# Performance work log

Measured on AMD Instinct MI355X. Metric: run time of the kernel, lower is better.

The kernel has to match this reference:

```python
import jax, jax.numpy as jnp
import numpy as np

B, T, D = 32, 2048, 1024
MAX_NSEG = 128  # max_nsegments
# max_nframes == T (required by the mask @ x matmul in the original module)


def setup_inputs() -> dict:
    key = jax.random.key(0)
    k1, k2 = jax.random.split(key)
    x = jax.random.normal(k1, (B, T, D), dtype=jnp.float32)
    # sparse segment boundaries, ~60 segments per utterance (< MAX_NSEG)
    in_boundary = (jax.random.uniform(k2, (B, T + 1)) < 0.03).astype(jnp.int32)
    # original code prepends 0 if first boundary != 0; also close the last segment
    in_boundary = in_boundary.at[:, 0].set(1).at[:, -1].set(1)
    return {"x": x, "in_boundary": in_boundary}


def _build_mask(in_boundary, n_seg, n_frames):
    # boundary at index i starts a new segment at frame i; index T only ends the
    # last segment, so frames 0..T-1 use boundary[:, :T]. Force a boundary at 0
    # (the original prepends 0 to segment_times when missing).
    b = in_boundary[:, :n_frames].at[:, 0].set(1)
    seg_id = jnp.cumsum(b, axis=1) - 1                       # [B, T] segment index per frame
    onehot = jax.nn.one_hot(seg_id, n_seg, dtype=jnp.float32)  # [B, T, S]; seg_id >= S -> all-zero row
    counts = onehot.sum(axis=1)                              # [B, S] frames per segment
    inv = jnp.where(counts > 0, 1.0 / jnp.maximum(counts, 1.0), 0.0)
    mask = jnp.swapaxes(onehot, 1, 2) * inv[:, :, None]      # [B, S, T], rows sum to 1 (or 0)
    return mask


def reference(x, in_boundary):
    mask = _build_mask(in_boundary, MAX_NSEG, x.shape[1])
    pooled = jnp.einsum('bst,btd->bsd', mask, x)             # segment mean-pooling
    return pooled, mask.sum(-1), in_boundary
```

## Files before the change

kernel.cpp:

```cpp
#include <hip/hip_runtime.h>

#define NB 32
#define NT 2048
#define ND 1024
#define NS 128
#define CH 64
#define NQ (NT / CH)

typedef float f32x4 __attribute__((ext_vector_type(4)));

__device__ __forceinline__ void nt_store4(float* p, float a, float b, float c, float d) {
    f32x4 v = {a, b, c, d};
    __builtin_nontemporal_store(v, (f32x4*)p);
}

__global__ __launch_bounds__(256)
void seg_scan_kernel(const int* __restrict__ in_boundary,
                     int* __restrict__ sid,
                     int* __restrict__ seg_start,
                     int* __restrict__ seg_count,
                     float* __restrict__ out1,
                     float* __restrict__ out2)
{
    const int b    = blockIdx.x;
    const int tid  = threadIdx.x;
    const int lane = tid & 63;
    const int wid  = tid >> 6;
    const int* bd  = in_boundary + (size_t)b * (NT + 1);

    __shared__ int starts[NS + 1];
    __shared__ int wtot[4];

    for (int s = tid; s <= NS; s += 256) starts[s] = NT;

    const int t0 = tid * 8;
    int v[8];
    int local = 0;
#pragma unroll
    for (int j = 0; j < 8; ++j) {
        int t = t0 + j;
        int bit = (t == 0) ? 1 : bd[t];
        v[j] = bit;
        local += bit;
    }

    int incl = local;
#pragma unroll
    for (int off = 1; off < 64; off <<= 1) {
        int n = __shfl_up(incl, off, 64);
        if (lane >= off) incl += n;
    }
    if (lane == 63) wtot[wid] = incl;
    __syncthreads();

    int wpref = 0;
#pragma unroll
    for (int w = 0; w < 4; ++w)
        if (w < wid) wpref += wtot[w];
    const int excl = wpref + incl - local;

    int run = excl;
#pragma unroll
    for (int j = 0; j < 8; ++j) {
        run += v[j];
        int seg = run - 1;
        sid[(size_t)b * NT + t0 + j] = seg;
        if (v[j] && seg <= NS) starts[seg] = t0 + j;
    }
    __syncthreads();

    if (tid < NS) {
        int st = starts[tid];
        int c  = starts[tid + 1] - st;
        seg_start[b * NS + tid] = st;
        seg_count[b * NS + tid] = c;
        out1[b * NS + tid] = (c > 0) ? 1.0f : 0.0f;
    }

    for (int t = tid; t <= NT; t += 256)
        out2[(size_t)b * (NT + 1) + t] = (float)bd[t];
}

__global__ __launch_bounds__(256)
void pool_chunk_kernel(const float* __restrict__ x,
                       const int* __restrict__ sid,
                       const int* __restrict__ seg_start,
                       const int* __restrict__ seg_count,
                       float* __restrict__ partial,
                       float* __restrict__ pooled)
{
    const int q   = blockIdx.x;
    const int b   = blockIdx.y;
    const int tid = threadIdx.x;
    const int t0  = q * CH;

    __shared__ int sid_l[CH];
    if (tid < CH) sid_l[tid] = sid[(size_t)b * NT + t0 + tid];
    __syncthreads();
    const int s_first = sid_l[0];

    const float4* xp = (const float4*)(x + (size_t)b * NT * ND) + tid;

    float4 acc = make_float4(0.f, 0.f, 0.f, 0.f);
    int cur = s_first;

    auto flush = [&](int seg, const float4& a) {
        if (seg >= NS) return;
        const int st = seg_start[b * NS + seg];
        const int c  = seg_count[b * NS + seg];
        if (st >= t0 && st + c <= t0 + CH) {
            const float inv = 1.0f / (float)c;
            nt_store4(pooled + ((size_t)b * NS + seg) * ND + tid * 4,
                      a.x * inv, a.y * inv, a.z * inv, a.w * inv);
        } else {
            const int slot = (seg == s_first) ? 0 : 1;
            ((float4*)partial)[(((size_t)b * NQ + q) * 2 + slot) * (ND / 4) + tid] = a;
        }
    };

    for (int g = 0; g < CH / 8; ++g) {
        float4 v[8];
#pragma unroll
        for (int j = 0; j < 8; ++j)
            v[j] = xp[(size_t)(t0 + g * 8 + j) * (ND / 4)];
#pragma unroll
        for (int j = 0; j < 8; ++j) {
            int sg = sid_l[g * 8 + j];
            if (sg != cur) {
                flush(cur, acc);
                acc = make_float4(0.f, 0.f, 0.f, 0.f);
                cur = sg;
            }
            acc.x += v[j].x; acc.y += v[j].y; acc.z += v[j].z; acc.w += v[j].w;
        }
    }
    flush(cur, acc);
}

__global__ __launch_bounds__(256)
void combine_kernel(const int* __restrict__ seg_start,
                    const int* __restrict__ seg_count,
                    const float* __restrict__ partial,
                    float* __restrict__ pooled)
{
    const int s   = blockIdx.x;
    const int b   = blockIdx.y;
    const int tid = threadIdx.x;

    const int st = seg_start[b * NS + s];
    const int c  = seg_count[b * NS + s];
    float* out = pooled + ((size_t)b * NS + s) * ND + tid * 4;

    if (c <= 0) {
        nt_store4(out, 0.f, 0.f, 0.f, 0.f);
        return;
    }
    const int q0 = st / CH;
    const int q1 = (st + c - 1) / CH;
    if (q0 == q1) return;

    const float4* pp = (const float4*)partial + tid;
    const int slot0 = (st == q0 * CH) ? 0 : 1;
    float4 a = pp[(((size_t)b * NQ + q0) * 2 + slot0) * (ND / 4)];
    for (int q = q0 + 1; q <= q1; ++q) {
        float4 v = pp[(((size_t)b * NQ + q) * 2 + 0) * (ND / 4)];
        a.x += v.x; a.y += v.y; a.z += v.z; a.w += v.w;
    }
    const float inv = 1.0f / (float)c;
    nt_store4(out, a.x * inv, a.y * inv, a.z * inv, a.w * inv);
}

extern "C" void kernel_launch(void* const* d_in, const int* in_sizes, int n_in,
                              void* d_out, int out_size, void* d_ws, size_t ws_size,
                              hipStream_t stream) {
    const float* x           = (const float*)d_in[0];
    const int*   in_boundary = (const int*)d_in[1];

    float* pooled = (float*)d_out;
    float* out1   = pooled + (size_t)NB * NS * ND;
    float* out2   = out1 + (size_t)NB * NS;

    int*   sid       = (int*)d_ws;
    int*   seg_start = sid + (size_t)NB * NT;
    int*   seg_count = seg_start + NB * NS;
    float* partial   = (float*)(seg_count + NB * NS);

    seg_scan_kernel<<<NB, 256, 0, stream>>>(in_boundary, sid, seg_start,
                                            seg_count, out1, out2);
    pool_chunk_kernel<<<dim3(NQ, NB), 256, 0, stream>>>(x, sid, seg_start,
                                                        seg_count, partial, pooled);
    combine_kernel<<<dim3(NS, NB), 256, 0, stream>>>(seg_start, seg_count,
                                                     partial, pooled);
}
```

Before: 56.30 us.

## Fuse segment scan into pooling kernel, recomputing scan per chunk block

```diff
diff --git a/kernel.cpp b/kernel.cpp
--- a/kernel.cpp
+++ b/kernel.cpp
@@ -15,32 +15,48 @@
 }
 
 __global__ __launch_bounds__(256)
-void seg_scan_kernel(const int* __restrict__ in_boundary,
-                     int* __restrict__ sid,
-                     int* __restrict__ seg_start,
-                     int* __restrict__ seg_count,
-                     float* __restrict__ out1,
-                     float* __restrict__ out2)
+void fused_pool_kernel(const float* __restrict__ x,
+                       const int* __restrict__ in_boundary,
+                       int* __restrict__ seg_start_ws,
+                       int* __restrict__ seg_count_ws,
+                       float* __restrict__ partial,
+                       float* __restrict__ pooled,
+                       float* __restrict__ out1,
+                       float* __restrict__ out2)
 {
-    const int b    = blockIdx.x;
+    const int q    = blockIdx.x;
+    const int b    = blockIdx.y;
     const int tid  = threadIdx.x;
     const int lane = tid & 63;
     const int wid  = tid >> 6;
+    const int t0   = q * CH;
     const int* bd  = in_boundary + (size_t)b * (NT + 1);
+
+    const float4* xp = (const float4*)(x + (size_t)b * NT * ND) + tid;
+
+    float4 p0 = xp[(size_t)(t0 + 0) * (ND / 4)];
+    float4 p1 = xp[(size_t)(t0 + 1) * (ND / 4)];
+    float4 p2 = xp[(size_t)(t0 + 2) * (ND / 4)];
+    float4 p3 = xp[(size_t)(t0 + 3) * (ND / 4)];
+    float4 p4 = xp[(size_t)(t0 + 4) * (ND / 4)];
+    float4 p5 = xp[(size_t)(t0 + 5) * (ND / 4)];
+    float4 p6 = xp[(size_t)(t0 + 6) * (ND / 4)];
+    float4 p7 = xp[(size_t)(t0 + 7) * (ND / 4)];
 
     __shared__ int starts[NS + 1];
     __shared__ int wtot[4];
+    __shared__ int sid_all[NT];
 
     for (int s = tid; s <= NS; s += 256) starts[s] = NT;
 
-    const int t0 = tid * 8;
-    int v[8];
+    const int f0 = tid * 8;
+    int bv[8];
     int local = 0;
 #pragma unroll
     for (int j = 0; j < 8; ++j) {
-        int t = t0 + j;
+        int t = f0 + j;
         int bit = (t == 0) ? 1 : bd[t];
-        v[j] = bit;
+        bv[j] = bit;
         local += bit;
     }
 
@@ -62,52 +78,33 @@
     int run = excl;
 #pragma unroll
     for (int j = 0; j < 8; ++j) {
-        run += v[j];
+        run += bv[j];
         int seg = run - 1;
-        sid[(size_t)b * NT + t0 + j] = seg;
-        if (v[j] && seg <= NS) starts[seg] = t0 + j;
+        sid_all[f0 + j] = seg;
+        if (bv[j] && seg <= NS) starts[seg] = f0 + j;
     }
     __syncthreads();
 
-    if (tid < NS) {
-        int st = starts[tid];
-        int c  = starts[tid + 1] - st;
-        seg_start[b * NS + tid] = st;
-        seg_count[b * NS + tid] = c;
-        out1[b * NS + tid] = (c > 0) ? 1.0f : 0.0f;
+    if (q == 0) {
+        if (tid < NS) {
+            int st = starts[tid];
+            int c  = starts[tid + 1] - st;
+            seg_start_ws[b * NS + tid] = st;
+            seg_count_ws[b * NS + tid] = c;
+            out1[b * NS + tid] = (c > 0) ? 1.0f : 0.0f;
+        }
+        for (int t = tid; t <= NT; t += 256)
+            out2[(size_t)b * (NT + 1) + t] = (float)bd[t];
     }
 
-    for (int t = tid; t <= NT; t += 256)
-        out2[(size_t)b * (NT + 1) + t] = (float)bd[t];
-}
-
-__global__ __launch_bounds__(256)
-void pool_chunk_kernel(const float* __restrict__ x,
-                       const int* __restrict__ sid,
-                       const int* __restrict__ seg_start,
-                       const int* __restrict__ seg_count,
-                       float* __restrict__ partial,
-                       float* __restrict__ pooled)
-{
-    const int q   = blockIdx.x;
-    const int b   = blockIdx.y;
-    const int tid = threadIdx.x;
-    const int t0  = q * CH;
-
-    __shared__ int sid_l[CH];
-    if (tid < CH) sid_l[tid] = sid[(size_t)b * NT + t0 + tid];
-    __syncthreads();
-    const int s_first = sid_l[0];
-
-    const float4* xp = (const float4*)(x + (size_t)b * NT * ND) + tid;
-
+    const int s_first = sid_all[t0];
     float4 acc = make_float4(0.f, 0.f, 0.f, 0.f);
     int cur = s_first;
 
     auto flush = [&](int seg, const float4& a) {
         if (seg >= NS) return;
-        const int st = seg_start[b * NS + seg];
-        const int c  = seg_count[b * NS + seg];
+        const int st = starts[seg];
+        const int c  = starts[seg + 1] - st;
         if (st >= t0 && st + c <= t0 + CH) {
             const float inv = 1.0f / (float)c;
             nt_store4(pooled + ((size_t)b * NS + seg) * ND + tid * 4,
@@ -118,21 +115,29 @@
         }
     };
 
-    for (int g = 0; g < CH / 8; ++g) {
+    auto consume = [&](int t, const float4& v) {
+        int sg = sid_all[t];
+        if (sg != cur) {
+            flush(cur, acc);
+            acc = make_float4(0.f, 0.f, 0.f, 0.f);
+            cur = sg;
+        }
+        acc.x += v.x; acc.y += v.y; acc.z += v.z; acc.w += v.w;
+    };
+
+    consume(t0 + 0, p0); consume(t0 + 1, p1);
+    consume(t0 + 2, p2); consume(t0 + 3, p3);
+    consume(t0 + 4, p4); consume(t0 + 5, p5);
+    consume(t0 + 6, p6); consume(t0 + 7, p7);
+
+    for (int g = 1; g < CH / 8; ++g) {
         float4 v[8];
 #pragma unroll
         for (int j = 0; j < 8; ++j)
             v[j] = xp[(size_t)(t0 + g * 8 + j) * (ND / 4)];
 #pragma unroll
-        for (int j = 0; j < 8; ++j) {
-            int sg = sid_l[g * 8 + j];
-            if (sg != cur) {
-                flush(cur, acc);
-                acc = make_float4(0.f, 0.f, 0.f, 0.f);
-                cur = sg;
-            }
-            acc.x += v[j].x; acc.y += v[j].y; acc.z += v[j].z; acc.w += v[j].w;
-        }
+        for (int j = 0; j < 8; ++j)
+            consume(t0 + g * 8 + j, v[j]);
     }
     flush(cur, acc);
 }
@@ -180,15 +185,12 @@
     float* out1   = pooled + (size_t)NB * NS * ND;
     float* out2   = out1 + (size_t)NB * NS;
 
-    int*   sid       = (int*)d_ws;
-    int*   seg_start = sid + (size_t)NB * NT;
+    int*   seg_start = (int*)d_ws;
     int*   seg_count = seg_start + NB * NS;
     float* partial   = (float*)(seg_count + NB * NS);
 
-    seg_scan_kernel<<<NB, 256, 0, stream>>>(in_boundary, sid, seg_start,
-                                            seg_count, out1, out2);
-    pool_chunk_kernel<<<dim3(NQ, NB), 256, 0, stream>>>(x, sid, seg_start,
-                                                        seg_count, partial, pooled);
+    fused_pool_kernel<<<dim3(NQ, NB), 256, 0, stream>>>(
+        x, in_boundary, seg_start, seg_count, partial, pooled, out1, out2);
     combine_kernel<<<dim3(NS, NB), 256, 0, stream>>>(seg_start, seg_count,
                                                      partial, pooled);
 }
```

Result: faster. 51.39 us (-8.7%).
